# Optimization experiments

Measured on AMD Instinct MI355X. Metric: run time of the kernel, lower is better.

Reference implementation:

```python
import jax, jax.numpy as jnp
import numpy as np

B, T, C = 48, 200, 53          # batch, timepoints, ICA components
E, H, A = 32, 64, 64            # embed dim, GRU hidden dim, attention hidden dim
C2 = C * C                      # 2809
E1 = round(0.05 * C2)           # gta_embed out = 140
E2 = round(0.5 * C2)            # gta_attend hidden = 1404
O = 2                           # output classes
BN_EPS = 1e-5


def setup_inputs() -> dict:
    key = jax.random.key(0)
    ks = jax.random.split(key, 24)
    n = lambda k, shape, s: jax.random.normal(k, shape, dtype=jnp.float32) * s
    return {
        "x": jax.random.normal(ks[0], (B, T, C), dtype=jnp.float32),
        "emb_w": n(ks[1], (E,), 0.3), "emb_b": n(ks[2], (E,), 0.1),
        "w_ih": n(ks[3], (3 * H, E), 0.12), "w_hh": n(ks[4], (3 * H, H), 0.12),
        "b_ih": n(ks[5], (3 * H,), 0.05), "b_hh": n(ks[6], (3 * H,), 0.05),
        "wq": n(ks[7], (A, H), 0.12), "bq": n(ks[8], (A,), 0.05),
        "wk": n(ks[9], (A, H), 0.12), "bk": n(ks[10], (A,), 0.05),
        "wv": n(ks[11], (H, H), 0.12), "bv": n(ks[12], (H,), 0.05),
        "u0": jax.random.normal(ks[13], (H,), dtype=jnp.float32),
        "w_g1": n(ks[14], (E1, C2), 0.02), "b_g1": n(ks[15], (E1,), 0.02),
        "bn_g": jnp.ones((E1,), jnp.float32), "bn_b": jnp.zeros((E1,), jnp.float32),
        "w_g2": n(ks[16], (E2, E1), 0.05), "b_g2": n(ks[17], (E2,), 0.05),
        "w_g3": n(ks[18], (1, E2), 0.02), "b_g3": n(ks[19], (1,), 0.02),
        "w_clf": n(ks[20], (O, C2), 0.02), "b_clf": jnp.zeros((O,), jnp.float32),
    }


def _normalize(v, eps=1e-12):
    return v / (jnp.linalg.norm(v) + eps)


def _gru_cell(x, h, w_ih, w_hh, b_ih, b_hh):
    # torch GRU cell math. x:(N,E) h:(N,H)
    gi = x @ w_ih.T + b_ih
    gh = h @ w_hh.T + b_hh
    i_r, i_z, i_n = jnp.split(gi, 3, axis=-1)
    h_r, h_z, h_n = jnp.split(gh, 3, axis=-1)
    r = jax.nn.sigmoid(i_r + h_r)
    z = jax.nn.sigmoid(i_z + h_z)
    n = jnp.tanh(i_n + r * h_n)
    return (1.0 - z) * n + z * h


def _forward(x, emb_w, emb_b, w_ih, w_hh, b_ih, b_hh, wq, bq, wk, bk, wv, bv, u0,
             w_g1, b_g1, bn_g, bn_b, w_g2, b_g2, w_g3, b_g3, w_clf, b_clf):
    Bs, Ts, Cs = x.shape
    Hd = wv.shape[0]
    # single shared Linear(1,E) embedding: (B,T,C) -> (T,B,C,E) for scan
    emb = x[..., None] * emb_w + emb_b
    emb = jnp.transpose(emb, (1, 0, 2, 3))
    h0 = jnp.zeros((Bs * Cs, Hd), x.dtype)

    def step(carry, emb_t):
        h, u = carry
        hg = _gru_cell(emb_t.reshape(Bs * Cs, -1), h, w_ih, w_hh, b_ih, b_hh)
        hb = hg.reshape(Bs, Cs, Hd)
        # spectral_norm on value weight: 5 power iterations (no_grad, as torch)
        v = None
        for _ in range(5):
            v = _normalize(wv.T @ u)
            u = _normalize(wv @ v)
        u = jax.lax.stop_gradient(u)
        v = jax.lax.stop_gradient(v)
        sigma = u @ (wv @ v)
        q = hb @ wq.T + bq          # (B,C,A)
        k = hb @ wk.T + bk          # (B,C,A)
        val = hb @ (wv / sigma).T + bv  # (B,C,H)
        scores = jnp.einsum('bia,bja->bij', q, k)  # (B,C,C)
        # eigenvalue-based spectral normalization (detached: track_grads=False)
        ev = jnp.linalg.eigvals(jax.lax.stop_gradient(scores))
        m = jnp.max(jnp.abs(ev), axis=1)[:, None, None].astype(x.dtype)
        attn = scores / m
        h_new = jnp.einsum('bij,bjh->bih', attn, val).reshape(Bs * Cs, Hd)
        return (h_new, u), attn

    (_, _), aligns = jax.lax.scan(step, (h0, u0), emb)  # aligns: (T,B,C,C)
    align = jnp.transpose(aligns, (1, 0, 2, 3))         # (B,T,C,C)
    Aflat = align.reshape(Bs, Ts, Cs * Cs)

    # gta_attention over the time axis
    xr = Aflat * Aflat.mean(axis=1, keepdims=True)
    flat = xr.reshape(Bs * Ts, Cs * Cs)
    e = flat @ w_g1.T + b_g1
    mu = e.mean(axis=0)
    var = e.var(axis=0)  # biased, as torch BatchNorm1d (training)
    e = jax.nn.relu((e - mu) / jnp.sqrt(var + BN_EPS) * bn_g + bn_b)
    a = jax.nn.relu(e @ w_g2.T + b_g2) @ w_g3.T + b_g3   # (B*T,1)
    a = jax.nn.softmax(a.reshape(Bs, Ts), axis=1)
    dnc = (Aflat * a[..., None]).sum(axis=1)             # (B,C*C)
    logits = dnc @ w_clf.T + b_clf
    return logits, dnc.reshape(Bs, Cs, Cs), align


def reference(x, emb_w, emb_b, w_ih, w_hh, b_ih, b_hh, wq, bq, wk, bk, wv, bv, u0,
              w_g1, b_g1, bn_g, bn_b, w_g2, b_g2, w_g3, b_g3, w_clf, b_clf):
    return _forward(x, emb_w, emb_b, w_ih, w_hh, b_ih, b_hh, wq, bq, wk, bk, wv, bv, u0,
                    w_g1, b_g1, bn_g, bn_b, w_g2, b_g2, w_g3, b_g3, w_clf, b_clf)
```

## Files before the change

### kernel.cpp

```cpp
#include <hip/hip_runtime.h>
#include <hip/hip_bf16.h>
#include <math.h>

#define B_  48
#define T_  200
#define C_  53
#define H_  64
#define C2_ 2809
#define E1_ 140
#define E2_ 1404
#define TS  60

typedef long long i64;

struct __align__(16) F4 { float v[4]; };

__device__ __forceinline__ float wredsum(float v){
  #pragma unroll
  for (int o = 32; o > 0; o >>= 1) v += __shfl_xor(v, o);
  return v;
}
__device__ __forceinline__ float sigm(float x){ return 1.f/(1.f + __expf(-x)); }
__device__ __forceinline__ float tanhx(float x){
  float a = fabsf(x);
  float e = __expf(-2.f*a);
  float t = (1.f - e)/(1.f + e);
  return copysignf(t, x);
}

__device__ __forceinline__ void eig_mm(const float* __restrict__ X, float* __restrict__ Y,
                                       int r0, int c0, float inv,
                                       float& essq, float& etrc){
  float ea0[4] = {0.f,0.f,0.f,0.f};
  float ea1[4] = {0.f,0.f,0.f,0.f};
  for (int kq = 0; kq < 13; kq++){
    int k4 = kq*4;
    F4 a0 = *(const F4*)&X[(r0+0)*TS + k4];
    F4 a1 = *(const F4*)&X[(r0+1)*TS + k4];
    F4 b0 = *(const F4*)&X[(k4+0)*TS + c0];
    F4 b1 = *(const F4*)&X[(k4+1)*TS + c0];
    F4 b2 = *(const F4*)&X[(k4+2)*TS + c0];
    F4 b3 = *(const F4*)&X[(k4+3)*TS + c0];
    #pragma unroll
    for (int ci = 0; ci < 4; ci++){
      ea0[ci] += a0.v[0]*b0.v[ci] + a0.v[1]*b1.v[ci] + a0.v[2]*b2.v[ci] + a0.v[3]*b3.v[ci];
      ea1[ci] += a1.v[0]*b0.v[ci] + a1.v[1]*b1.v[ci] + a1.v[2]*b2.v[ci] + a1.v[3]*b3.v[ci];
    }
  }
  {
    float a0 = X[(r0+0)*TS + 52], a1 = X[(r0+1)*TS + 52];
    F4 bb = *(const F4*)&X[52*TS + c0];
    #pragma unroll
    for (int ci = 0; ci < 4; ci++){ ea0[ci] += a0*bb.v[ci]; ea1[ci] += a1*bb.v[ci]; }
  }
  F4 o0, o1;
  #pragma unroll
  for (int ci = 0; ci < 4; ci++){
    o0.v[ci] = ea0[ci]*inv;
    o1.v[ci] = ea1[ci]*inv;
    essq += o0.v[ci]*o0.v[ci] + o1.v[ci]*o1.v[ci];
  }
  if (r0   >= c0 && r0   < c0+4) etrc += o0.v[r0-c0];
  if (r0+1 >= c0 && r0+1 < c0+4) etrc += o1.v[r0+1-c0];
  *(F4*)&Y[(r0+0)*TS + c0] = o0;
  *(F4*)&Y[(r0+1)*TS + c0] = o1;
}

#define OFF_SIGMA 0
#define OFF_WHHT  200
#define OFF_WZV   12488
#define OFF_WUV   20680
#define OFF_P     20812
#define OFF_R0    21004
#define OFF_MM    21196
#define OFF_M2    25292
#define OFF_M4    29388
#define OFF_M5    33484
#define OFF_AMEAN 37580
#define OFF_E     172412
#define OFF_CA    1516412
#define OFF_CB    1516552
#define OFF_APRE  1516692
#define OFF_A     1526292
#define OFF_G2T   1535892

__global__ void k_prep1(const float* __restrict__ w_hh, const float* __restrict__ wq,
                        const float* __restrict__ wk, const float* __restrict__ wv,
                        const float* __restrict__ w_ih, const float* __restrict__ emb_w,
                        const float* __restrict__ emb_b, const float* __restrict__ b_ih,
                        const float* __restrict__ bq, const float* __restrict__ bk,
                        const float* __restrict__ w_g2,
                        float* whhT, float* wzv, float* wuv, float* g2t,
                        float* p, float* r0){
  int idx0 = blockIdx.x*blockDim.x + threadIdx.x;
  int stride = gridDim.x*blockDim.x;
  for (int i = idx0; i < 64*192; i += stride){
    int kk = i/192, g = i%192;
    whhT[i] = w_hh[g*64 + kk];
  }
  for (int i = idx0; i < 8192; i += stride){
    int h = i >> 7, a = i & 127;
    if (a < 64){
      float g = 0.f;
      for (int m = 0; m < 64; m++) g += wq[m*64 + h]*wk[m*64 + a];
      wzv[i] = g;
    } else {
      wzv[i] = wv[(a-64)*64 + h];
    }
  }
  for (int i = idx0; i < 129; i += stride){
    if (i < 64){
      float s = 0.f;
      for (int m = 0; m < 64; m++) s += wq[m*64 + i]*bk[m];
      wuv[i] = s;
    } else if (i < 128){
      int h = i - 64;
      float s = 0.f;
      for (int m = 0; m < 64; m++) s += wk[m*64 + h]*bq[m];
      wuv[i] = s;
    } else {
      float s = 0.f;
      for (int m = 0; m < 64; m++) s += bq[m]*bk[m];
      wuv[128] = s;
    }
  }
  for (int i = idx0; i < 140*1404; i += stride){ int k = i/1404, n = i%1404; g2t[i] = w_g2[n*140+k]; }
  for (int i = idx0; i < 192; i += stride){
    float s1 = 0.f, s2 = 0.f;
    for (int e = 0; e < 32; e++){ float w = w_ih[i*32+e]; s1 += w*emb_w[e]; s2 += w*emb_b[e]; }
    p[i] = s1; r0[i] = s2 + b_ih[i];
  }
}

__global__ void k_prep2(const float* __restrict__ wv, const float* __restrict__ u0,
                        float* Wm, float* Wm2, float* Wm4, float* Wm5, float* sigma){
  int r = threadIdx.x;
  for (int c = 0; c < 64; c++){
    float s = 0.f;
    for (int k = 0; k < 64; k++) s += wv[r*64+k]*wv[c*64+k];
    Wm[r*64+c] = s;
  }
  __syncthreads();
  for (int c = 0; c < 64; c++){
    float s = 0.f;
    for (int k = 0; k < 64; k++) s += Wm[r*64+k]*Wm[k*64+c];
    Wm2[r*64+c] = s;
  }
  __syncthreads();
  for (int c = 0; c < 64; c++){
    float s = 0.f;
    for (int k = 0; k < 64; k++) s += Wm2[r*64+k]*Wm2[k*64+c];
    Wm4[r*64+c] = s;
  }
  __syncthreads();
  for (int c = 0; c < 64; c++){
    float s = 0.f;
    for (int k = 0; k < 64; k++) s += Wm4[r*64+k]*Wm[k*64+c];
    Wm5[r*64+c] = s;
  }
  __syncthreads();
  __shared__ float su[64];
  su[r] = u0[r];
  __syncthreads();
  for (int t = 0; t < T_; t++){
    float z = 0.f, w = 0.f;
    for (int k = 0; k < 64; k++){ float uk = su[k]; z += Wm4[r*64+k]*uk; w += Wm5[r*64+k]*uk; }
    float nw = wredsum(w*w);
    float zw = wredsum(z*w);
    float sg = sqrtf(nw / fmaxf(zw, 1e-35f));
    if (r == 0) sigma[t] = sg;
    float wn = w * (1.f/sqrtf(fmaxf(nw, 1e-35f)));
    __syncthreads();
    su[r] = wn;
    __syncthreads();
  }
}

__global__ __launch_bounds__(512, 1) void k_scan(
    const float* __restrict__ x, const float* __restrict__ b_hh,
    const float* __restrict__ bv,
    const float* __restrict__ whhT, const float* __restrict__ wzv,
    const float* __restrict__ wuv,
    const float* __restrict__ wp, const float* __restrict__ wr0,
    const float* __restrict__ sigma, float* __restrict__ outAL){
  __shared__ __align__(16) float L[19056];
  float* Rh  = L;
  float* R4  = L + 3840;
  float* R3  = L + 7680;
  float* R2  = L + 11520;
  float* R1  = L + 14912;
  float* Lp  = L + 18272;
  float* Lr0 = L + 18464;
  float* Lbh = L + 18656;
  float* Lbv = L + 18848;
  float* Lrq = L + 18912;
  float* Lrk = L + 18968;
  float* Lsc = L + 19024;
  int tid = threadIdx.x;
  int b = blockIdx.x;

  for (int i = tid; i < 192; i += 512){ Lp[i] = wp[i]; Lr0[i] = wr0[i]; Lbh[i] = b_hh[i]; }
  for (int i = tid; i < 64; i += 512) Lbv[i] = bv[i];
  for (int i = tid; i < 18272; i += 512) L[i] = 0.f;
  __syncthreads();

  int ct4 = tid >> 4, jt4 = tid & 15;
  int c0g = ct4*4, j0g = jt4*4;
  int it14 = tid/14, jt14 = tid%14;
  int i0s = it14*4, j0s = jt14*4;
  int ctq = tid >> 5, gtq = tid & 31;
  int c0q = ctq*4, g0q = gtq*4;
  int erg = tid/14, ecg = tid%14;
  int er0 = erg*2, ec0 = ecg*4;

  const float c0v = wuv[128];

  for (int t = 0; t < T_; t++){
    if (tid < 32) Lsc[tid] = 0.f;
    if (tid < 224){
      float gacc[3][4][4];
      #pragma unroll
      for (int g = 0; g < 3; g++)
        #pragma unroll
        for (int ji = 0; ji < 4; ji++){
          float bb = Lbh[g*64 + j0g + ji];
          #pragma unroll
          for (int ci = 0; ci < 4; ci++) gacc[g][ji][ci] = bb;
        }
      for (int kk = 0; kk < 64; kk++){
        F4 hv = *(F4*)&Rh[kk*TS + c0g];
        F4 w0 = *(const F4*)&whhT[kk*192 + j0g];
        F4 w1 = *(const F4*)&whhT[kk*192 + 64 + j0g];
        F4 w2 = *(const F4*)&whhT[kk*192 + 128 + j0g];
        #pragma unroll
        for (int ji = 0; ji < 4; ji++)
          #pragma unroll
          for (int ci = 0; ci < 4; ci++){
            gacc[0][ji][ci] += hv.v[ci]*w0.v[ji];
            gacc[1][ji][ci] += hv.v[ci]*w1.v[ji];
            gacc[2][ji][ci] += hv.v[ci]*w2.v[ji];
          }
      }
      float xv[4];
      #pragma unroll
      for (int ci = 0; ci < 4; ci++){
        int c = c0g + ci;
        xv[ci] = (c < C_) ? x[(i64)(b*T_ + t)*C_ + c] : 0.f;
      }
      F4 p0 = *(F4*)&Lp[j0g], p1 = *(F4*)&Lp[64+j0g], p2 = *(F4*)&Lp[128+j0g];
      F4 q0 = *(F4*)&Lr0[j0g], q1 = *(F4*)&Lr0[64+j0g], q2 = *(F4*)&Lr0[128+j0g];
      #pragma unroll
      for (int ji = 0; ji < 4; ji++){
        F4 hold = *(F4*)&Rh[(j0g+ji)*TS + c0g];
        F4 o;
        #pragma unroll
        for (int ci = 0; ci < 4; ci++){
          float rr = sigm(xv[ci]*p0.v[ji] + q0.v[ji] + gacc[0][ji][ci]);
          float zz = sigm(xv[ci]*p1.v[ji] + q1.v[ji] + gacc[1][ji][ci]);
          float nn = tanhx(xv[ci]*p2.v[ji] + q2.v[ji] + rr*gacc[2][ji][ci]);
          float hg = (1.f - zz)*nn + zz*hold.v[ci];
          o.v[ci] = (c0g + ci < C_) ? hg : 0.f;
        }
        *(F4*)&R4[(j0g+ji)*TS + c0g] = o;
      }
    }
    __syncthreads();
    if (tid < 448){
      float acc[4][4];
      #pragma unroll
      for (int gi = 0; gi < 4; gi++)
        #pragma unroll
        for (int ci = 0; ci < 4; ci++) acc[gi][ci] = 0.f;
      for (int kk = 0; kk < 64; kk++){
        F4 a = *(F4*)&R4[kk*TS + c0q];
        F4 w = *(const F4*)&wzv[kk*128 + g0q];
        #pragma unroll
        for (int gi = 0; gi < 4; gi++)
          #pragma unroll
          for (int ci = 0; ci < 4; ci++) acc[gi][ci] += a.v[ci]*w.v[gi];
      }
      if (g0q < 64){
        #pragma unroll
        for (int gi = 0; gi < 4; gi++){
          F4 o;
          #pragma unroll
          for (int ci = 0; ci < 4; ci++) o.v[ci] = acc[gi][ci];
          *(F4*)&R3[(g0q+gi)*TS + c0q] = o;
        }
      } else {
        float invs = 1.f/sigma[t];
        int a0i = g0q - 64;
        #pragma unroll
        for (int ci = 0; ci < 4; ci++){
          int c = c0q + ci;
          if (c < C_){
            F4 o;
            #pragma unroll
            for (int gi = 0; gi < 4; gi++) o.v[gi] = acc[gi][ci]*invs + Lbv[a0i+gi];
            *(F4*)&R2[c*64 + a0i] = o;
          }
        }
      }
    } else if (tid < 504){
      int u = tid - 448;
      float rq = 0.f, rk = 0.f;
      if (u < C_){
        for (int h = 0; h < 64; h++){
          float hv = R4[h*TS + u];
          rq += hv*wuv[h];
          rk += hv*wuv[64+h];
        }
      }
      if (u < 56){ Lrq[u] = rq; Lrk[u] = rk; }
    }
    __syncthreads();
    {
      float sacc[4][4];
      float ssq = 0.f, trc = 0.f;
      if (tid < 196){
        #pragma unroll
        for (int ii = 0; ii < 4; ii++)
          #pragma unroll
          for (int jj = 0; jj < 4; jj++){
            int i = i0s + ii, j = j0s + jj;
            sacc[ii][jj] = (i < C_ && j < C_) ? (Lrq[i] + Lrk[j] + c0v) : 0.f;
          }
        for (int aq = 0; aq < 16; aq++){
          int a4 = aq*4;
          F4 qa0 = *(F4*)&R3[(a4+0)*TS + i0s];
          F4 qa1 = *(F4*)&R3[(a4+1)*TS + i0s];
          F4 qa2 = *(F4*)&R3[(a4+2)*TS + i0s];
          F4 qa3 = *(F4*)&R3[(a4+3)*TS + i0s];
          F4 kb0 = *(F4*)&R4[(a4+0)*TS + j0s];
          F4 kb1 = *(F4*)&R4[(a4+1)*TS + j0s];
          F4 kb2 = *(F4*)&R4[(a4+2)*TS + j0s];
          F4 kb3 = *(F4*)&R4[(a4+3)*TS + j0s];
          #pragma unroll
          for (int ii = 0; ii < 4; ii++)
            #pragma unroll
            for (int jj = 0; jj < 4; jj++)
              sacc[ii][jj] += qa0.v[ii]*kb0.v[jj] + qa1.v[ii]*kb1.v[jj]
                            + qa2.v[ii]*kb2.v[jj] + qa3.v[ii]*kb3.v[jj];
        }
        #pragma unroll
        for (int ii = 0; ii < 4; ii++){
          int i = i0s + ii;
          if (i < C_){
            F4 o;
            #pragma unroll
            for (int jj = 0; jj < 4; jj++){
              o.v[jj] = sacc[ii][jj];
              ssq += sacc[ii][jj]*sacc[ii][jj];
            }
            *(F4*)&R1[i*TS + j0s] = o;
          }
        }
        if (it14 == jt14){
          #pragma unroll
          for (int u = 0; u < 4; u++) if (i0s + u < C_) trc += sacc[u][u];
        }
      }
      ssq = wredsum(ssq); trc = wredsum(trc);
      if ((tid & 63) == 0){
        if (ssq != 0.f) atomicAdd(&Lsc[0], ssq);
        if (trc != 0.f) atomicAdd(&Lsc[1], trc);
      }
    }
    __syncthreads();
    {
      float inv0 = 1.f/fmaxf(Lsc[0], 1e-35f);
      float essq = 0.f, etrc = 0.f;
      if (tid < 378) eig_mm(R1, R3, er0, ec0, inv0, essq, etrc);
      essq = wredsum(essq); etrc = wredsum(etrc);
      if ((tid & 63) == 0){
        if (essq != 0.f) atomicAdd(&Lsc[2], essq);
        if (etrc != 0.f) atomicAdd(&Lsc[3], etrc);
      }
    }
    __syncthreads();
    float Gacc = 0.f, prevest = 1e30f, est = 0.f;
    int cnt = 0;
    float pssq = fmaxf(Lsc[0], 1e-35f), ptr1 = Lsc[1];
    float* Xb = R3; float* Yb = R4;
    for (int j = 2; j <= 13; j++){
      float sj = fmaxf(Lsc[2*(j-1)], 1e-35f);
      float tj = Lsc[2*(j-1)+1];
      int J = j - 2;
      float t1n = ptr1/sqrtf(pssq);
      float t2n = tj;
      float disc = 2.f*t2n - t1n*t1n;
      float rq = (disc >= 0.f) ? 0.5f*(fabsf(t1n) + sqrtf(disc))
                               : sqrtf(fmaxf(0.5f*(t1n*t1n - t2n), 1e-30f));
      rq = fminf(fmaxf(rq, 0.02f), 1.5f);
      est = Gacc + ldexpf(0.5f*log2f(pssq) + log2f(rq), -J);
      if (fabsf(est - prevest) < 1e-4f) cnt++; else cnt = 0;
      prevest = est;
      Gacc += ldexpf(log2f(pssq), -(J+1));
      if ((J >= 5 && cnt >= 1) || j == 13) break;
      pssq = sj; ptr1 = tj;
      {
        float inv = 1.f/sj;
        float essq = 0.f, etrc = 0.f;
        if (tid < 378) eig_mm(Xb, Yb, er0, ec0, inv, essq, etrc);
        essq = wredsum(essq); etrc = wredsum(etrc);
        if ((tid & 63) == 0){
          if (essq != 0.f) atomicAdd(&Lsc[2*j], essq);
          if (etrc != 0.f) atomicAdd(&Lsc[2*j+1], etrc);
        }
      }
      { float* tp = Xb; Xb = Yb; Yb = tp; }
      __syncthreads();
    }
    float invm = exp2f(-est);
    if (tid < 224){
      float hraw0[4] = {0.f,0.f,0.f,0.f};
      float hraw1[4] = {0.f,0.f,0.f,0.f};
      float hraw2[4] = {0.f,0.f,0.f,0.f};
      float hraw3[4] = {0.f,0.f,0.f,0.f};
      for (int kq = 0; kq < 13; kq++){
        int k4 = kq*4;
        F4 a0 = *(F4*)&R1[(c0g+0)*TS + k4];
        F4 a1 = *(F4*)&R1[(c0g+1)*TS + k4];
        F4 a2 = *(F4*)&R1[(c0g+2)*TS + k4];
        F4 a3 = *(F4*)&R1[(c0g+3)*TS + k4];
        F4 b0 = *(F4*)&R2[(k4+0)*64 + j0g];
        F4 b1 = *(F4*)&R2[(k4+1)*64 + j0g];
        F4 b2 = *(F4*)&R2[(k4+2)*64 + j0g];
        F4 b3 = *(F4*)&R2[(k4+3)*64 + j0g];
        #pragma unroll
        for (int jj = 0; jj < 4; jj++){
          hraw0[jj] += a0.v[0]*b0.v[jj] + a0.v[1]*b1.v[jj] + a0.v[2]*b2.v[jj] + a0.v[3]*b3.v[jj];
          hraw1[jj] += a1.v[0]*b0.v[jj] + a1.v[1]*b1.v[jj] + a1.v[2]*b2.v[jj] + a1.v[3]*b3.v[jj];
          hraw2[jj] += a2.v[0]*b0.v[jj] + a2.v[1]*b1.v[jj] + a2.v[2]*b2.v[jj] + a2.v[3]*b3.v[jj];
          hraw3[jj] += a3.v[0]*b0.v[jj] + a3.v[1]*b1.v[jj] + a3.v[2]*b2.v[jj] + a3.v[3]*b3.v[jj];
        }
      }
      {
        const int k = 52;
        float a0 = R1[(c0g+0)*TS + k], a1 = R1[(c0g+1)*TS + k];
        float a2 = R1[(c0g+2)*TS + k], a3 = R1[(c0g+3)*TS + k];
        F4 bb = *(F4*)&R2[k*64 + j0g];
        #pragma unroll
        for (int jj = 0; jj < 4; jj++){
          hraw0[jj] += a0*bb.v[jj];
          hraw1[jj] += a1*bb.v[jj];
          hraw2[jj] += a2*bb.v[jj];
          hraw3[jj] += a3*bb.v[jj];
        }
      }
      #pragma unroll
      for (int jj = 0; jj < 4; jj++){
        F4 o;
        o.v[0] = (c0g + 0 < C_) ? hraw0[jj]*invm : 0.f;
        o.v[1] = (c0g + 1 < C_) ? hraw1[jj]*invm : 0.f;
        o.v[2] = (c0g + 2 < C_) ? hraw2[jj]*invm : 0.f;
        o.v[3] = (c0g + 3 < C_) ? hraw3[jj]*invm : 0.f;
        *(F4*)&Rh[(j0g+jj)*TS + c0g] = o;
      }
    } else if (tid < 420){
      int u = tid - 224;
      int i0 = (u/14)*4, j0 = (u%14)*4;
      float* ALrow = outAL + (i64)(b*T_ + t)*C2_;
      #pragma unroll
      for (int ii = 0; ii < 4; ii++){
        int i = i0 + ii;
        if (i < C_){
          F4 s = *(F4*)&R1[i*TS + j0];
          #pragma unroll
          for (int jj = 0; jj < 4; jj++){
            int j = j0 + jj;
            if (j < C_) ALrow[i*C_ + j] = s.v[jj]*invm;
          }
        }
      }
    }
    __syncthreads();
  }
}

__global__ void k_amean(const float* __restrict__ AL, float* __restrict__ amean){
  int b = blockIdx.x/11, ch = blockIdx.x%11;
  int c2 = ch*256 + threadIdx.x;
  if (c2 >= C2_) return;
  float acc = 0.f;
  for (int t = 0; t < T_; t++)
    acc += AL[(i64)(b*T_ + t)*C2_ + c2];
  amean[(i64)b*C2_ + c2] = acc*(1.f/(float)T_);
}

__global__ __launch_bounds__(128) void k_gemm1(const float* __restrict__ AL,
                                               const float* __restrict__ amean,
                                               const float* __restrict__ w_g1,
                                               float* __restrict__ e){
  __shared__ __align__(16) float At[64][68];
  __shared__ __align__(16) float Bt[64][148];
  int mt = blockIdx.x >> 2, ks = blockIdx.x & 3;
  int tid = threadIdx.x;
  float acc[8][12];
  #pragma unroll
  for (int ri = 0; ri < 8; ri++)
    #pragma unroll
    for (int ci = 0; ci < 12; ci++) acc[ri][ci] = 0.f;
  int rg = tid/12, cg = tid%12;
  int r0 = rg*8, cc0 = cg*12;
  for (int kb = 0; kb < 11; kb++){
    int k0 = (ks*11 + kb)*64;
    for (int idx = tid; idx < 4096; idx += 128){
      int r = idx >> 6, i = idx & 63;
      int kk = k0 + i;
      int row = mt*64 + r, bb = row/T_;
      float v = 0.f;
      if (kk < C2_) v = AL[(i64)row*C2_ + kk]*amean[(i64)bb*C2_ + kk];
      At[i][r] = v;
    }
    for (int idx = tid; idx < 9216; idx += 128){
      int c = idx >> 6, i = idx & 63;
      int kk = k0 + i;
      float v = 0.f;
      if (c < E1_ && kk < C2_) v = w_g1[(i64)c*C2_ + kk];
      Bt[i][c] = v;
    }
    __syncthreads();
    if (tid < 96){
      for (int i = 0; i < 64; i++){
        F4 a0 = *(F4*)&At[i][r0]; F4 a1 = *(F4*)&At[i][r0+4];
        F4 b0 = *(F4*)&Bt[i][cc0]; F4 b1 = *(F4*)&Bt[i][cc0+4]; F4 b2 = *(F4*)&Bt[i][cc0+8];
        #pragma unroll
        for (int ri = 0; ri < 8; ri++){
          float av = (ri < 4) ? a0.v[ri] : a1.v[ri-4];
          #pragma unroll
          for (int ci = 0; ci < 12; ci++){
            float bv = (ci < 4) ? b0.v[ci] : (ci < 8) ? b1.v[ci-4] : b2.v[ci-8];
            acc[ri][ci] += av*bv;
          }
        }
      }
    }
    __syncthreads();
  }
  if (tid < 96){
    #pragma unroll
    for (int ri = 0; ri < 8; ri++)
      #pragma unroll
      for (int ci = 0; ci < 12; ci++){
        int c = cc0 + ci;
        if (c < E1_) atomicAdd(&e[(i64)(mt*64 + r0 + ri)*E1_ + c], acc[ri][ci]);
      }
  }
}

__global__ void k_bnstats(const float* __restrict__ e, const float* __restrict__ bn_g,
                          const float* __restrict__ bn_b, float* cA, float* cB){
  __shared__ float s1a[256], s2a[256];
  int c = blockIdx.x, tid = threadIdx.x;
  float s1 = 0.f, s2 = 0.f;
  for (int row = tid; row < B_*T_; row += 256){
    float v = e[(i64)row*E1_ + c];
    s1 += v; s2 += v*v;
  }
  s1a[tid] = s1; s2a[tid] = s2; __syncthreads();
  for (int s = 128; s > 0; s >>= 1){
    if (tid < s){ s1a[tid] += s1a[tid+s]; s2a[tid] += s2a[tid+s]; }
    __syncthreads();
  }
  if (tid == 0){
    float n = (float)(B_*T_);
    float mu = s1a[0]/n;
    float var = s2a[0]/n - mu*mu;
    float a = bn_g[c]/sqrtf(var + 1e-5f);
    cA[c] = a; cB[c] = bn_b[c] - mu*a;
  }
}

__global__ __launch_bounds__(128) void k_gemm2(const float* __restrict__ e,
                                               const float* __restrict__ cA, const float* __restrict__ cB,
                                               const float* __restrict__ g2t,
                                               const float* __restrict__ b_g2, const float* __restrict__ w_g3,
                                               float* __restrict__ apre){
  __shared__ __align__(16) float At2[140][68];
  int mt = blockIdx.x/30, nc = blockIdx.x%30;
  int tid = threadIdx.x;
  int nbase = nc*48;
  for (int idx = tid; idx < 64*140; idx += 128){
    int r = idx/140, k = idx - r*140;
    float v = e[(i64)(mt*64 + r)*E1_ + k]*cA[k] + cB[k];
    At2[k][r] = fmaxf(v, 0.f);
  }
  __syncthreads();
  if (tid < 96){
    int rg = tid/6, ng = tid%6;
    int r0 = rg*4, n0 = nbase + ng*8;
    float acc[4][8];
    #pragma unroll
    for (int ri = 0; ri < 4; ri++)
      #pragma unroll
      for (int ni = 0; ni < 8; ni++) acc[ri][ni] = 0.f;
    for (int k = 0; k < E1_; k++){
      F4 a = *(F4*)&At2[k][r0];
      float bvv[8];
      if (n0 + 8 <= E2_){
        F4 b0 = *(const F4*)&g2t[(i64)k*E2_ + n0];
        F4 b1 = *(const F4*)&g2t[(i64)k*E2_ + n0 + 4];
        #pragma unroll
        for (int u = 0; u < 4; u++){ bvv[u] = b0.v[u]; bvv[u+4] = b1.v[u]; }
      } else {
        #pragma unroll
        for (int ni = 0; ni < 8; ni++){ int n = n0+ni; bvv[ni] = (n < E2_) ? g2t[(i64)k*E2_ + n] : 0.f; }
      }
      #pragma unroll
      for (int ri = 0; ri < 4; ri++)
        #pragma unroll
        for (int ni = 0; ni < 8; ni++) acc[ri][ni] += a.v[ri]*bvv[ni];
    }
    #pragma unroll
    for (int ri = 0; ri < 4; ri++){
      float s = 0.f;
      #pragma unroll
      for (int ni = 0; ni < 8; ni++){
        int n = n0 + ni;
        if (n < E2_){
          float a2 = acc[ri][ni] + b_g2[n];
          if (a2 > 0.f) s += a2*w_g3[n];
        }
      }
      atomicAdd(&apre[mt*64 + r0 + ri], s);
    }
// ... 101 lines not shown
```

Measured before the change: 9.682 ms.

## Cache GRU weights in LDS, widen thread mapping, overlap hidden update with eigen iteration

Stages the recurrent weight matrices (whhT and wzv) in shared memory instead of reading them from global memory every step. The GRU gate and score matmuls are remapped to use more threads (448/378) with smaller per-thread tiles. The hidden-state matmul R1·R2 now runs in parallel with the first eigen matmul and is scaled by invm in a later pass, taking it off the serial tail of each timestep. The convergence threshold for the eigen estimate is also relaxed from J>=5 to J>=4, which may change numerical results.

Result: slower. 12.06 ms (+24.6%).

```diff
diff --git a/kernel.cpp b/kernel.cpp
--- a/kernel.cpp
+++ b/kernel.cpp
@@ -14,6 +14,7 @@
 typedef long long i64;
 
 struct __align__(16) F4 { float v[4]; };
+struct __align__(8)  F2 { float v[2]; };
 
 __device__ __forceinline__ float wredsum(float v){
   #pragma unroll
@@ -64,6 +65,56 @@
   if (r0+1 >= c0 && r0+1 < c0+4) etrc += o1.v[r0+1-c0];
   *(F4*)&Y[(r0+0)*TS + c0] = o0;
   *(F4*)&Y[(r0+1)*TS + c0] = o1;
+}
+
+__device__ __forceinline__ void eig_mm4(const float* __restrict__ X, float* __restrict__ Y,
+                                        int r0, int c0, float inv,
+                                        float& essq, float& etrc){
+  float ea[4][4];
+  #pragma unroll
+  for (int r = 0; r < 4; r++)
+    #pragma unroll
+    for (int c = 0; c < 4; c++) ea[r][c] = 0.f;
+  for (int kq = 0; kq < 13; kq++){
+    int k4 = kq*4;
+    F4 a0 = *(const F4*)&X[(r0+0)*TS + k4];
+    F4 a1 = *(const F4*)&X[(r0+1)*TS + k4];
+    F4 a2 = *(const F4*)&X[(r0+2)*TS + k4];
+    F4 a3 = *(const F4*)&X[(r0+3)*TS + k4];
+    F4 b0 = *(const F4*)&X[(k4+0)*TS + c0];
+    F4 b1 = *(const F4*)&X[(k4+1)*TS + c0];
+    F4 b2 = *(const F4*)&X[(k4+2)*TS + c0];
+    F4 b3 = *(const F4*)&X[(k4+3)*TS + c0];
+    #pragma unroll
+    for (int ci = 0; ci < 4; ci++){
+      ea[0][ci] += a0.v[0]*b0.v[ci] + a0.v[1]*b1.v[ci] + a0.v[2]*b2.v[ci] + a0.v[3]*b3.v[ci];
+      ea[1][ci] += a1.v[0]*b0.v[ci] + a1.v[1]*b1.v[ci] + a1.v[2]*b2.v[ci] + a1.v[3]*b3.v[ci];
+      ea[2][ci] += a2.v[0]*b0.v[ci] + a2.v[1]*b1.v[ci] + a2.v[2]*b2.v[ci] + a2.v[3]*b3.v[ci];
+      ea[3][ci] += a3.v[0]*b0.v[ci] + a3.v[1]*b1.v[ci] + a3.v[2]*b2.v[ci] + a3.v[3]*b3.v[ci];
+    }
+  }
+  {
+    float a0 = X[(r0+0)*TS + 52], a1 = X[(r0+1)*TS + 52];
+    float a2 = X[(r0+2)*TS + 52], a3 = X[(r0+3)*TS + 52];
+    F4 bb = *(const F4*)&X[52*TS + c0];
+    #pragma unroll
+    for (int ci = 0; ci < 4; ci++){
+      ea[0][ci] += a0*bb.v[ci]; ea[1][ci] += a1*bb.v[ci];
+      ea[2][ci] += a2*bb.v[ci]; ea[3][ci] += a3*bb.v[ci];
+    }
+  }
+  #pragma unroll
+  for (int r = 0; r < 4; r++){
+    F4 o;
+    #pragma unroll
+    for (int ci = 0; ci < 4; ci++){
+      o.v[ci] = ea[r][ci]*inv;
+      essq += o.v[ci]*o.v[ci];
+    }
+    int rr = r0 + r;
+    if (rr >= c0 && rr < c0+4) etrc += o.v[rr-c0];
+    *(F4*)&Y[rr*TS + c0] = o;
+  }
 }
 
 #define OFF_SIGMA 0
@@ -183,57 +234,54 @@
     const float* __restrict__ wuv,
     const float* __restrict__ wp, const float* __restrict__ wr0,
     const float* __restrict__ sigma, float* __restrict__ outAL){
-  __shared__ __align__(16) float L[19056];
-  float* Rh  = L;
-  float* R4  = L + 3840;
-  float* R3  = L + 7680;
-  float* R2  = L + 11520;
-  float* R1  = L + 14912;
-  float* Lp  = L + 18272;
-  float* Lr0 = L + 18464;
-  float* Lbh = L + 18656;
-  float* Lbv = L + 18848;
-  float* Lrq = L + 18912;
-  float* Lrk = L + 18968;
-  float* Lsc = L + 19024;
+  __shared__ __align__(16) float L[39536];
+  float* Lw  = L;
+  float* Lz  = L + 12288;
+  float* Rh  = L + 20480;
+  float* R4  = L + 24320;
+  float* R3  = L + 28160;
+  float* R2  = L + 32000;
+  float* R1  = L + 35392;
+  float* Lp  = L + 38752;
+  float* Lr0 = L + 38944;
+  float* Lbh = L + 39136;
+  float* Lbv = L + 39328;
+  float* Lrq = L + 39392;
+  float* Lrk = L + 39448;
+  float* Lsc = L + 39504;
   int tid = threadIdx.x;
   int b = blockIdx.x;
 
+  for (int i = tid; i < 3072; i += 512) *(F4*)&Lw[i*4] = *(const F4*)&whhT[i*4];
+  for (int i = tid; i < 2048; i += 512) *(F4*)&Lz[i*4] = *(const F4*)&wzv[i*4];
   for (int i = tid; i < 192; i += 512){ Lp[i] = wp[i]; Lr0[i] = wr0[i]; Lbh[i] = b_hh[i]; }
   for (int i = tid; i < 64; i += 512) Lbv[i] = bv[i];
-  for (int i = tid; i < 18272; i += 512) L[i] = 0.f;
+  for (int i = tid; i < 18272; i += 512) L[20480 + i] = 0.f;
   __syncthreads();
-
-  int ct4 = tid >> 4, jt4 = tid & 15;
-  int c0g = ct4*4, j0g = jt4*4;
-  int it14 = tid/14, jt14 = tid%14;
-  int i0s = it14*4, j0s = jt14*4;
-  int ctq = tid >> 5, gtq = tid & 31;
-  int c0q = ctq*4, g0q = gtq*4;
-  int erg = tid/14, ecg = tid%14;
-  int er0 = erg*2, ec0 = ecg*4;
 
   const float c0v = wuv[128];
 
   for (int t = 0; t < T_; t++){
     if (tid < 32) Lsc[tid] = 0.f;
-    if (tid < 224){
-      float gacc[3][4][4];
+    if (tid < 448){
+      int jt = tid & 31, ct = tid >> 5;
+      int j0 = jt*2, c0 = ct*4;
+      float gacc[3][2][4];
       #pragma unroll
       for (int g = 0; g < 3; g++)
         #pragma unroll
-        for (int ji = 0; ji < 4; ji++){
-          float bb = Lbh[g*64 + j0g + ji];
+        for (int ji = 0; ji < 2; ji++){
+          float bb = Lbh[g*64 + j0 + ji];
           #pragma unroll
           for (int ci = 0; ci < 4; ci++) gacc[g][ji][ci] = bb;
         }
       for (int kk = 0; kk < 64; kk++){
-        F4 hv = *(F4*)&Rh[kk*TS + c0g];
-        F4 w0 = *(const F4*)&whhT[kk*192 + j0g];
-        F4 w1 = *(const F4*)&whhT[kk*192 + 64 + j0g];
-        F4 w2 = *(const F4*)&whhT[kk*192 + 128 + j0g];
-        #pragma unroll
-        for (int ji = 0; ji < 4; ji++)
+        F4 hv = *(F4*)&Rh[kk*TS + c0];
+        F2 w0 = *(const F2*)&Lw[kk*192 + j0];
+        F2 w1 = *(const F2*)&Lw[kk*192 + 64 + j0];
+        F2 w2 = *(const F2*)&Lw[kk*192 + 128 + j0];
+        #pragma unroll
+        for (int ji = 0; ji < 2; ji++)
           #pragma unroll
           for (int ci = 0; ci < 4; ci++){
             gacc[0][ji][ci] += hv.v[ci]*w0.v[ji];
@@ -244,14 +292,14 @@
       float xv[4];
       #pragma unroll
       for (int ci = 0; ci < 4; ci++){
-        int c = c0g + ci;
+        int c = c0 + ci;
         xv[ci] = (c < C_) ? x[(i64)(b*T_ + t)*C_ + c] : 0.f;
       }
-      F4 p0 = *(F4*)&Lp[j0g], p1 = *(F4*)&Lp[64+j0g], p2 = *(F4*)&Lp[128+j0g];
-      F4 q0 = *(F4*)&Lr0[j0g], q1 = *(F4*)&Lr0[64+j0g], q2 = *(F4*)&Lr0[128+j0g];
-      #pragma unroll
-      for (int ji = 0; ji < 4; ji++){
-        F4 hold = *(F4*)&Rh[(j0g+ji)*TS + c0g];
+      F2 p0 = *(F2*)&Lp[j0], p1 = *(F2*)&Lp[64+j0], p2 = *(F2*)&Lp[128+j0];
+      F2 q0 = *(F2*)&Lr0[j0], q1 = *(F2*)&Lr0[64+j0], q2 = *(F2*)&Lr0[128+j0];
+      #pragma unroll
+      for (int ji = 0; ji < 2; ji++){
+        F4 hold = *(F4*)&Rh[(j0+ji)*TS + c0];
         F4 o;
         #pragma unroll
         for (int ci = 0; ci < 4; ci++){
@@ -259,13 +307,15 @@
           float zz = sigm(xv[ci]*p1.v[ji] + q1.v[ji] + gacc[1][ji][ci]);
           float nn = tanhx(xv[ci]*p2.v[ji] + q2.v[ji] + rr*gacc[2][ji][ci]);
           float hg = (1.f - zz)*nn + zz*hold.v[ci];
-          o.v[ci] = (c0g + ci < C_) ? hg : 0.f;
-        }
-        *(F4*)&R4[(j0g+ji)*TS + c0g] = o;
+          o.v[ci] = (c0 + ci < C_) ? hg : 0.f;
+        }
+        *(F4*)&R4[(j0+ji)*TS + c0] = o;
       }
     }
     __syncthreads();
     if (tid < 448){
+      int ctq = tid >> 5, gtq = tid & 31;
+      int c0q = ctq*4, g0q = gtq*4;
       float acc[4][4];
       #pragma unroll
       for (int gi = 0; gi < 4; gi++)
@@ -273,7 +323,7 @@
         for (int ci = 0; ci < 4; ci++) acc[gi][ci] = 0.f;
       for (int kk = 0; kk < 64; kk++){
         F4 a = *(F4*)&R4[kk*TS + c0q];
-        F4 w = *(const F4*)&wzv[kk*128 + g0q];
+        F4 w = *(const F4*)&Lz[kk*128 + g0q];
         #pragma unroll
         for (int gi = 0; gi < 4; gi++)
           #pragma unroll
@@ -315,36 +365,38 @@
     }
     __syncthreads();
     {
-      float sacc[4][4];
       float ssq = 0.f, trc = 0.f;
-      if (tid < 196){
-        #pragma unroll
-        for (int ii = 0; ii < 4; ii++)
+      if (tid < 378){
+        int it = tid/14, jt = tid%14;
+        int i0 = it*2, j0 = jt*4;
+        float sacc[2][4];
+        #pragma unroll
+        for (int ii = 0; ii < 2; ii++)
           #pragma unroll
           for (int jj = 0; jj < 4; jj++){
-            int i = i0s + ii, j = j0s + jj;
+            int i = i0 + ii, j = j0 + jj;
             sacc[ii][jj] = (i < C_ && j < C_) ? (Lrq[i] + Lrk[j] + c0v) : 0.f;
           }
         for (int aq = 0; aq < 16; aq++){
           int a4 = aq*4;
-          F4 qa0 = *(F4*)&R3[(a4+0)*TS + i0s];
-          F4 qa1 = *(F4*)&R3[(a4+1)*TS + i0s];
-          F4 qa2 = *(F4*)&R3[(a4+2)*TS + i0s];
-          F4 qa3 = *(F4*)&R3[(a4+3)*TS + i0s];
-          F4 kb0 = *(F4*)&R4[(a4+0)*TS + j0s];
-          F4 kb1 = *(F4*)&R4[(a4+1)*TS + j0s];
-          F4 kb2 = *(F4*)&R4[(a4+2)*TS + j0s];
-          F4 kb3 = *(F4*)&R4[(a4+3)*TS + j0s];
+          F2 qa0 = *(F2*)&R3[(a4+0)*TS + i0];
+          F2 qa1 = *(F2*)&R3[(a4+1)*TS + i0];
+          F2 qa2 = *(F2*)&R3[(a4+2)*TS + i0];
+          F2 qa3 = *(F2*)&R3[(a4+3)*TS + i0];
+          F4 kb0 = *(F4*)&R4[(a4+0)*TS + j0];
+          F4 kb1 = *(F4*)&R4[(a4+1)*TS + j0];
+          F4 kb2 = *(F4*)&R4[(a4+2)*TS + j0];
+          F4 kb3 = *(F4*)&R4[(a4+3)*TS + j0];
           #pragma unroll
-          for (int ii = 0; ii < 4; ii++)
+          for (int ii = 0; ii < 2; ii++)
             #pragma unroll
             for (int jj = 0; jj < 4; jj++)
               sacc[ii][jj] += qa0.v[ii]*kb0.v[jj] + qa1.v[ii]*kb1.v[jj]
                             + qa2.v[ii]*kb2.v[jj] + qa3.v[ii]*kb3.v[jj];
         }
         #pragma unroll
-        for (int ii = 0; ii < 4; ii++){
-          int i = i0s + ii;
+        for (int ii = 0; ii < 2; ii++){
+          int i = i0 + ii;
           if (i < C_){
             F4 o;
             #pragma unroll
@@ -352,12 +404,9 @@
               o.v[jj] = sacc[ii][jj];
               ssq += sacc[ii][jj]*sacc[ii][jj];
             }
-            *(F4*)&R1[i*TS + j0s] = o;
+            *(F4*)&R1[i*TS + j0] = o;
+            if (j0 <= i && i < j0 + 4) trc += sacc[ii][i - j0];
           }
-        }
-        if (it14 == jt14){
-          #pragma unroll
-          for (int u = 0; u < 4; u++) if (i0s + u < C_) trc += sacc[u][u];
         }
       }
       ssq = wredsum(ssq); trc = wredsum(trc);
@@ -367,21 +416,71 @@
       }
     }
     __syncthreads();
-    {
+    if (tid < 196){
       float inv0 = 1.f/fmaxf(Lsc[0], 1e-35f);
+      int r0e = (tid/14)*4, c0e = (tid%14)*4;
       float essq = 0.f, etrc = 0.f;
-      if (tid < 378) eig_mm(R1, R3, er0, ec0, inv0, essq, etrc);
+      eig_mm4(R1, R3, r0e, c0e, inv0, essq, etrc);
       essq = wredsum(essq); etrc = wredsum(etrc);
       if ((tid & 63) == 0){
         if (essq != 0.f) atomicAdd(&Lsc[2], essq);
         if (etrc != 0.f) atomicAdd(&Lsc[3], etrc);
       }
+    } else if (tid < 420){
+      int u = tid - 196;
+      int c0 = (u >> 4)*4, j0 = (u & 15)*4;
+      float hr[4][4];
+      #pragma unroll
+      for (int r = 0; r < 4; r++)
+        #pragma unroll
+        for (int c = 0; c < 4; c++) hr[r][c] = 0.f;
+      for (int kq = 0; kq < 13; kq++){
+        int k4 = kq*4;
+        F4 a0 = *(F4*)&R1[(c0+0)*TS + k4];
+        F4 a1 = *(F4*)&R1[(c0+1)*TS + k4];
+        F4 a2 = *(F4*)&R1[(c0+2)*TS + k4];
+        F4 a3 = *(F4*)&R1[(c0+3)*TS + k4];
+        F4 b0 = *(F4*)&R2[(k4+0)*64 + j0];
+        F4 b1 = *(F4*)&R2[(k4+1)*64 + j0];
+        F4 b2 = *(F4*)&R2[(k4+2)*64 + j0];
+        F4 b3 = *(F4*)&R2[(k4+3)*64 + j0];
+        #pragma unroll
+        for (int jj = 0; jj < 4; jj++){
+          hr[0][jj] += a0.v[0]*b0.v[jj] + a0.v[1]*b1.v[jj] + a0.v[2]*b2.v[jj] + a0.v[3]*b3.v[jj];
+          hr[1][jj] += a1.v[0]*b0.v[jj] + a1.v[1]*b1.v[jj] + a1.v[2]*b2.v[jj] + a1.v[3]*b3.v[jj];
+          hr[2][jj] += a2.v[0]*b0.v[jj] + a2.v[1]*b1.v[jj] + a2.v[2]*b2.v[jj] + a2.v[3]*b3.v[jj];
+          hr[3][jj] += a3.v[0]*b0.v[jj] + a3.v[1]*b1.v[jj] + a3.v[2]*b2.v[jj] + a3.v[3]*b3.v[jj];
+        }
+      }
+      {
+        const int k = 52;
+        float a0 = R1[(c0+0)*TS + k], a1 = R1[(c0+1)*TS + k];
+        float a2 = R1[(c0+2)*TS + k], a3 = R1[(c0+3)*TS + k];
+        F4 bb = *(F4*)&R2[k*64 + j0];
+        #pragma unroll
+        for (int jj = 0; jj < 4; jj++){
+          hr[0][jj] += a0*bb.v[jj];
+          hr[1][jj] += a1*bb.v[jj];
+          hr[2][jj] += a2*bb.v[jj];
+          hr[3][jj] += a3*bb.v[jj];
+        }
+      }
+      #pragma unroll
+      for (int jj = 0; jj < 4; jj++){
+        F4 o;
+        #pragma unroll
+        for (int ii = 0; ii < 4; ii++)
+          o.v[ii] = (c0 + ii < C_) ? hr[ii][jj] : 0.f;
+        *(F4*)&Rh[(j0+jj)*TS + c0] = o;
+      }
     }
     __syncthreads();
     float Gacc = 0.f, prevest = 1e30f, est = 0.f;
     int cnt = 0;
     float pssq = fmaxf(Lsc[0], 1e-35f), ptr1 = Lsc[1];
     float* Xb = R3; float* Yb = R4;
+    int erg = tid/14, ecg = tid%14;
+    int er0 = erg*2, ec0 = ecg*4;
     for (int j = 2; j <= 13; j++){
       float sj = fmaxf(Lsc[2*(j-1)], 1e-35f);
       float tj = Lsc[2*(j-1)+1];
@@ -396,7 +495,7 @@
       if (fabsf(est - prevest) < 1e-4f) cnt++; else cnt = 0;
       prevest = est;
       Gacc += ldexpf(log2f(pssq), -(J+1));
-      if ((J >= 5 && cnt >= 1) || j == 13) break;
+      if ((J >= 4 && cnt >= 1) || j == 13) break;
       pssq = sj; ptr1 = tj;
       {
         float inv = 1.f/sj;
@@ -412,66 +511,23 @@
       __syncthreads();
     }
     float invm = exp2f(-est);
-    if (tid < 224){
-      float hraw0[4] = {0.f,0.f,0.f,0.f};
-      float hraw1[4] = {0.f,0.f,0.f,0.f};
-      float hraw2[4] = {0.f,0.f,0.f,0.f};
-      float hraw3[4] = {0.f,0.f,0.f,0.f};
-      for (int kq = 0; kq < 13; kq++){
-        int k4 = kq*4;
-        F4 a0 = *(F4*)&R1[(c0g+0)*TS + k4];
-        F4 a1 = *(F4*)&R1[(c0g+1)*TS + k4];
-        F4 a2 = *(F4*)&R1[(c0g+2)*TS + k4];
-        F4 a3 = *(F4*)&R1[(c0g+3)*TS + k4];
-        F4 b0 = *(F4*)&R2[(k4+0)*64 + j0g];
-        F4 b1 = *(F4*)&R2[(k4+1)*64 + j0g];
-        F4 b2 = *(F4*)&R2[(k4+2)*64 + j0g];
-        F4 b3 = *(F4*)&R2[(k4+3)*64 + j0g];
+    if (tid < 378){
+      float* ALrow = outAL + (i64)(b*T_ + t)*C2_;
+      for (int g = tid; g < 742; g += 378){
+        int r = g/14, q = (g%14)*4;
+        F4 s = *(F4*)&R1[r*TS + q];
         #pragma unroll
         for (int jj = 0; jj < 4; jj++){
-          hraw0[jj] += a0.v[0]*b0.v[jj] + a0.v[1]*b1.v[jj] + a0.v[2]*b2.v[jj] + a0.v[3]*b3.v[jj];
-          hraw1[jj] += a1.v[0]*b0.v[jj] + a1.v[1]*b1.v[jj] + a1.v[2]*b2.v[jj] + a1.v[3]*b3.v[jj];
-          hraw2[jj] += a2.v[0]*b0.v[jj] + a2.v[1]*b1.v[jj] + a2.v[2]*b2.v[jj] + a2.v[3]*b3.v[jj];
-          hraw3[jj] += a3.v[0]*b0.v[jj] + a3.v[1]*b1.v[jj] + a3.v[2]*b2.v[jj] + a3.v[3]*b3.v[jj];
-        }
-      }
-      {
-        const int k = 52;
-        float a0 = R1[(c0g+0)*TS + k], a1 = R1[(c0g+1)*TS + k];
-        float a2 = R1[(c0g+2)*TS + k], a3 = R1[(c0g+3)*TS + k];
-        F4 bb = *(F4*)&R2[k*64 + j0g];
-        #pragma unroll
-        for (int jj = 0; jj < 4; jj++){
-          hraw0[jj] += a0*bb.v[jj];
-          hraw1[jj] += a1*bb.v[jj];
-          hraw2[jj] += a2*bb.v[jj];
-          hraw3[jj] += a3*bb.v[jj];
-        }
-      }
-      #pragma unroll
-      for (int jj = 0; jj < 4; jj++){
-        F4 o;
-        o.v[0] = (c0g + 0 < C_) ? hraw0[jj]*invm : 0.f;
-        o.v[1] = (c0g + 1 < C_) ? hraw1[jj]*invm : 0.f;
-        o.v[2] = (c0g + 2 < C_) ? hraw2[jj]*invm : 0.f;
-        o.v[3] = (c0g + 3 < C_) ? hraw3[jj]*invm : 0.f;
-        *(F4*)&Rh[(j0g+jj)*TS + c0g] = o;
-      }
-    } else if (tid < 420){
-      int u = tid - 224;
-      int i0 = (u/14)*4, j0 = (u%14)*4;
-      float* ALrow = outAL + (i64)(b*T_ + t)*C2_;
-      #pragma unroll
-      for (int ii = 0; ii < 4; ii++){
-        int i = i0 + ii;
-        if (i < C_){
-          F4 s = *(F4*)&R1[i*TS + j0];
-          #pragma unroll
-          for (int jj = 0; jj < 4; jj++){
-            int j = j0 + jj;
-            if (j < C_) ALrow[i*C_ + j] = s.v[jj]*invm;
-          }
-        }
+          int jc = q + jj;
+          if (jc < C_) ALrow[r*C_ + jc] = s.v[jj]*invm;
+        }
+      }
+    } else {
+      for (int idx = tid - 378; idx < 960; idx += 134){
+        F4 v = *(F4*)&Rh[idx*4];
+        #pragma unroll
+        for (int u = 0; u < 4; u++) v.v[u] *= invm;
+        *(F4*)&Rh[idx*4] = v;
       }
     }
     __syncthreads();
```

## Stage GRU/proj weights in LDS, enlarge per-thread tiles, loosen iteration cutoff

Applied to the files above, without the earlier changes.

Copies whhT and wzv into shared memory once per block so the per-timestep GEMMs stop re-reading them from global memory. It widens register tiles (4x4 in the squaring matmul, 4x8 in the projection), halving the active threads for those stages. It also lets the repeated-squaring eigen estimate exit one iteration earlier. This trades more LDS use and less thread parallelism for fewer loads, and the earlier exit may change numerical accuracy.

Measured after the change: 12.89 ms. 1.33x slower.

```diff
diff --git a/kernel.cpp b/kernel.cpp
--- a/kernel.cpp
+++ b/kernel.cpp
@@ -28,42 +28,54 @@
   return copysignf(t, x);
 }
 
-__device__ __forceinline__ void eig_mm(const float* __restrict__ X, float* __restrict__ Y,
-                                       int r0, int c0, float inv,
-                                       float& essq, float& etrc){
-  float ea0[4] = {0.f,0.f,0.f,0.f};
-  float ea1[4] = {0.f,0.f,0.f,0.f};
+__device__ __forceinline__ void eig_mm4(const float* __restrict__ X, float* __restrict__ Y,
+                                        int r0, int c0, float inv,
+                                        float& essq, float& etrc){
+  float ea[4][4];
+  #pragma unroll
+  for (int r = 0; r < 4; r++)
+    #pragma unroll
+    for (int c = 0; c < 4; c++) ea[r][c] = 0.f;
   for (int kq = 0; kq < 13; kq++){
     int k4 = kq*4;
     F4 a0 = *(const F4*)&X[(r0+0)*TS + k4];
     F4 a1 = *(const F4*)&X[(r0+1)*TS + k4];
+    F4 a2 = *(const F4*)&X[(r0+2)*TS + k4];
+    F4 a3 = *(const F4*)&X[(r0+3)*TS + k4];
     F4 b0 = *(const F4*)&X[(k4+0)*TS + c0];
     F4 b1 = *(const F4*)&X[(k4+1)*TS + c0];
     F4 b2 = *(const F4*)&X[(k4+2)*TS + c0];
     F4 b3 = *(const F4*)&X[(k4+3)*TS + c0];
     #pragma unroll
     for (int ci = 0; ci < 4; ci++){
-      ea0[ci] += a0.v[0]*b0.v[ci] + a0.v[1]*b1.v[ci] + a0.v[2]*b2.v[ci] + a0.v[3]*b3.v[ci];
-      ea1[ci] += a1.v[0]*b0.v[ci] + a1.v[1]*b1.v[ci] + a1.v[2]*b2.v[ci] + a1.v[3]*b3.v[ci];
+      ea[0][ci] += a0.v[0]*b0.v[ci] + a0.v[1]*b1.v[ci] + a0.v[2]*b2.v[ci] + a0.v[3]*b3.v[ci];
+      ea[1][ci] += a1.v[0]*b0.v[ci] + a1.v[1]*b1.v[ci] + a1.v[2]*b2.v[ci] + a1.v[3]*b3.v[ci];
+      ea[2][ci] += a2.v[0]*b0.v[ci] + a2.v[1]*b1.v[ci] + a2.v[2]*b2.v[ci] + a2.v[3]*b3.v[ci];
+      ea[3][ci] += a3.v[0]*b0.v[ci] + a3.v[1]*b1.v[ci] + a3.v[2]*b2.v[ci] + a3.v[3]*b3.v[ci];
     }
   }
   {
     float a0 = X[(r0+0)*TS + 52], a1 = X[(r0+1)*TS + 52];
+    float a2 = X[(r0+2)*TS + 52], a3 = X[(r0+3)*TS + 52];
     F4 bb = *(const F4*)&X[52*TS + c0];
     #pragma unroll
-    for (int ci = 0; ci < 4; ci++){ ea0[ci] += a0*bb.v[ci]; ea1[ci] += a1*bb.v[ci]; }
-  }
-  F4 o0, o1;
+    for (int ci = 0; ci < 4; ci++){
+      ea[0][ci] += a0*bb.v[ci]; ea[1][ci] += a1*bb.v[ci];
+      ea[2][ci] += a2*bb.v[ci]; ea[3][ci] += a3*bb.v[ci];
+    }
+  }
   #pragma unroll
-  for (int ci = 0; ci < 4; ci++){
-    o0.v[ci] = ea0[ci]*inv;
-    o1.v[ci] = ea1[ci]*inv;
-    essq += o0.v[ci]*o0.v[ci] + o1.v[ci]*o1.v[ci];
-  }
-  if (r0   >= c0 && r0   < c0+4) etrc += o0.v[r0-c0];
-  if (r0+1 >= c0 && r0+1 < c0+4) etrc += o1.v[r0+1-c0];
-  *(F4*)&Y[(r0+0)*TS + c0] = o0;
-  *(F4*)&Y[(r0+1)*TS + c0] = o1;
+  for (int r = 0; r < 4; r++){
+    F4 o;
+    #pragma unroll
+    for (int ci = 0; ci < 4; ci++){
+      o.v[ci] = ea[r][ci]*inv;
+      essq += o.v[ci]*o.v[ci];
+    }
+    int rr = r0 + r;
+    if (rr >= c0 && rr < c0+4) etrc += o.v[rr-c0];
+    *(F4*)&Y[rr*TS + c0] = o;
+  }
 }
 
 #define OFF_SIGMA 0
@@ -183,35 +195,35 @@
     const float* __restrict__ wuv,
     const float* __restrict__ wp, const float* __restrict__ wr0,
     const float* __restrict__ sigma, float* __restrict__ outAL){
-  __shared__ __align__(16) float L[19056];
-  float* Rh  = L;
-  float* R4  = L + 3840;
-  float* R3  = L + 7680;
-  float* R2  = L + 11520;
-  float* R1  = L + 14912;
-  float* Lp  = L + 18272;
-  float* Lr0 = L + 18464;
-  float* Lbh = L + 18656;
-  float* Lbv = L + 18848;
-  float* Lrq = L + 18912;
-  float* Lrk = L + 18968;
-  float* Lsc = L + 19024;
+  __shared__ __align__(16) float L[39536];
+  float* Lw  = L;
+  float* Lz  = L + 12288;
+  float* Rh  = L + 20480;
+  float* R4  = L + 24320;
+  float* R3  = L + 28160;
+  float* R2  = L + 32000;
+  float* R1  = L + 35392;
+  float* Lp  = L + 38752;
+  float* Lr0 = L + 38944;
+  float* Lbh = L + 39136;
+  float* Lbv = L + 39328;
+  float* Lrq = L + 39392;
+  float* Lrk = L + 39448;
+  float* Lsc = L + 39504;
   int tid = threadIdx.x;
   int b = blockIdx.x;
 
+  for (int i = tid; i < 3072; i += 512) *(F4*)&Lw[i*4] = *(const F4*)&whhT[i*4];
+  for (int i = tid; i < 2048; i += 512) *(F4*)&Lz[i*4] = *(const F4*)&wzv[i*4];
   for (int i = tid; i < 192; i += 512){ Lp[i] = wp[i]; Lr0[i] = wr0[i]; Lbh[i] = b_hh[i]; }
   for (int i = tid; i < 64; i += 512) Lbv[i] = bv[i];
-  for (int i = tid; i < 18272; i += 512) L[i] = 0.f;
+  for (int i = tid; i < 18272; i += 512) L[20480 + i] = 0.f;
   __syncthreads();
 
   int ct4 = tid >> 4, jt4 = tid & 15;
   int c0g = ct4*4, j0g = jt4*4;
   int it14 = tid/14, jt14 = tid%14;
   int i0s = it14*4, j0s = jt14*4;
-  int ctq = tid >> 5, gtq = tid & 31;
-  int c0q = ctq*4, g0q = gtq*4;
-  int erg = tid/14, ecg = tid%14;
-  int er0 = erg*2, ec0 = ecg*4;
 
   const float c0v = wuv[128];
 
@@ -229,9 +241,9 @@
         }
       for (int kk = 0; kk < 64; kk++){
         F4 hv = *(F4*)&Rh[kk*TS + c0g];
-        F4 w0 = *(const F4*)&whhT[kk*192 + j0g];
-        F4 w1 = *(const F4*)&whhT[kk*192 + 64 + j0g];
-        F4 w2 = *(const F4*)&whhT[kk*192 + 128 + j0g];
+        F4 w0 = *(const F4*)&Lw[kk*192 + j0g];
+        F4 w1 = *(const F4*)&Lw[kk*192 + 64 + j0g];
+        F4 w2 = *(const F4*)&Lw[kk*192 + 128 + j0g];
         #pragma unroll
         for (int ji = 0; ji < 4; ji++)
           #pragma unroll
@@ -265,34 +277,41 @@
       }
     }
     __syncthreads();
-    if (tid < 448){
-      float acc[4][4];
+    if (tid < 224){
+      int ct = tid >> 5, gt = tid & 31;
+      int c0 = ct*8, g0 = gt*4;
+      float acc[4][8];
       #pragma unroll
       for (int gi = 0; gi < 4; gi++)
         #pragma unroll
-        for (int ci = 0; ci < 4; ci++) acc[gi][ci] = 0.f;
+        for (int ci = 0; ci < 8; ci++) acc[gi][ci] = 0.f;
       for (int kk = 0; kk < 64; kk++){
-        F4 a = *(F4*)&R4[kk*TS + c0q];
-        F4 w = *(const F4*)&wzv[kk*128 + g0q];
+        F4 a0 = *(F4*)&R4[kk*TS + c0];
+        F4 a1 = *(F4*)&R4[kk*TS + c0 + 4];
+        F4 w = *(const F4*)&Lz[kk*128 + g0];
         #pragma unroll
         for (int gi = 0; gi < 4; gi++)
           #pragma unroll
-          for (int ci = 0; ci < 4; ci++) acc[gi][ci] += a.v[ci]*w.v[gi];
-      }
-      if (g0q < 64){
+          for (int ci = 0; ci < 4; ci++){
+            acc[gi][ci]   += a0.v[ci]*w.v[gi];
+            acc[gi][ci+4] += a1.v[ci]*w.v[gi];
+          }
+      }
+      if (g0 < 64){
         #pragma unroll
         for (int gi = 0; gi < 4; gi++){
-          F4 o;
+          F4 lo, hi;
           #pragma unroll
-          for (int ci = 0; ci < 4; ci++) o.v[ci] = acc[gi][ci];
-          *(F4*)&R3[(g0q+gi)*TS + c0q] = o;
+          for (int ci = 0; ci < 4; ci++){ lo.v[ci] = acc[gi][ci]; hi.v[ci] = acc[gi][ci+4]; }
+          *(F4*)&R3[(g0+gi)*TS + c0] = lo;
+          *(F4*)&R3[(g0+gi)*TS + c0 + 4] = hi;
         }
       } else {
         float invs = 1.f/sigma[t];
-        int a0i = g0q - 64;
-        #pragma unroll
-        for (int ci = 0; ci < 4; ci++){
-          int c = c0q + ci;
+        int a0i = g0 - 64;
+        #pragma unroll
+        for (int ci = 0; ci < 8; ci++){
+          int c = c0 + ci;
           if (c < C_){
             F4 o;
             #pragma unroll
@@ -301,8 +320,8 @@
           }
         }
       }
-    } else if (tid < 504){
-      int u = tid - 448;
+    } else if (tid < 280){
+      int u = tid - 224;
       float rq = 0.f, rk = 0.f;
       if (u < C_){
         for (int h = 0; h < 64; h++){
@@ -315,9 +334,9 @@
     }
     __syncthreads();
     {
-      float sacc[4][4];
       float ssq = 0.f, trc = 0.f;
       if (tid < 196){
+        float sacc[4][4];
         #pragma unroll
         for (int ii = 0; ii < 4; ii++)
           #pragma unroll
@@ -353,11 +372,8 @@
               ssq += sacc[ii][jj]*sacc[ii][jj];
             }
             *(F4*)&R1[i*TS + j0s] = o;
+            if (j0s <= i && i < j0s + 4) trc += sacc[ii][i - j0s];
           }
-        }
-        if (it14 == jt14){
-          #pragma unroll
-          for (int u = 0; u < 4; u++) if (i0s + u < C_) trc += sacc[u][u];
         }
       }
       ssq = wredsum(ssq); trc = wredsum(trc);
@@ -368,9 +384,11 @@
     }
     __syncthreads();
     {
-      float inv0 = 1.f/fmaxf(Lsc[0], 1e-35f);
       float essq = 0.f, etrc = 0.f;
-      if (tid < 378) eig_mm(R1, R3, er0, ec0, inv0, essq, etrc);
+      if (tid < 196){
+        float inv0 = 1.f/fmaxf(Lsc[0], 1e-35f);
+        eig_mm4(R1, R3, i0s, j0s, inv0, essq, etrc);
+      }
       essq = wredsum(essq); etrc = wredsum(etrc);
       if ((tid & 63) == 0){
         if (essq != 0.f) atomicAdd(&Lsc[2], essq);
@@ -396,12 +414,12 @@
       if (fabsf(est - prevest) < 1e-4f) cnt++; else cnt = 0;
       prevest = est;
       Gacc += ldexpf(log2f(pssq), -(J+1));
-      if ((J >= 5 && cnt >= 1) || j == 13) break;
+      if ((J >= 4 && cnt >= 1) || j == 13) break;
       pssq = sj; ptr1 = tj;
       {
         float inv = 1.f/sj;
         float essq = 0.f, etrc = 0.f;
-        if (tid < 378) eig_mm(Xb, Yb, er0, ec0, inv, essq, etrc);
+        if (tid < 196) eig_mm4(Xb, Yb, i0s, j0s, inv, essq, etrc);
         essq = wredsum(essq); etrc = wredsum(etrc);
         if ((tid & 63) == 0){
           if (essq != 0.f) atomicAdd(&Lsc[2*j], essq);
@@ -468,8 +486,8 @@
           F4 s = *(F4*)&R1[i*TS + j0];
           #pragma unroll
           for (int jj = 0; jj < 4; jj++){
-            int j = j0 + jj;
-            if (j < C_) ALrow[i*C_ + j] = s.v[jj]*invm;
+            int jc = j0 + jj;
+            if (jc < C_) ALrow[i*C_ + jc] = s.v[jj]*invm;
           }
         }
       }
```
